# Optimization experiments

Hardware: AMD Instinct MI355X
Metric: run time of the kernel (lower is better)

The kernel has to match this reference:

```python
import jax, jax.numpy as jnp
import numpy as np

N, D, E, H, K = 16384, 256, 8, 512, 2


def setup_inputs() -> dict:
    key = jax.random.key(0)
    ks = jax.random.split(key, 5)
    inputs = jax.random.normal(ks[0], (N, D), dtype=jnp.float32)
    Wg = jax.random.normal(ks[1], (D, E), dtype=jnp.float32) * 0.05
    w1 = jax.random.normal(ks[2], (E, D, H), dtype=jnp.float32) * 0.05
    b1 = jnp.zeros((E, H), dtype=jnp.float32)
    w2 = jax.random.normal(ks[3], (E, H, D), dtype=jnp.float32) * 0.05
    b2 = jnp.zeros((E, D), dtype=jnp.float32)
    return {"inputs": inputs, "Wg": Wg, "w1": w1, "b1": b1, "w2": w2, "b2": b2}


def reference(inputs, Wg, w1, b1, w2, b2):
    # gate + top-k routing (softmax over the selected logits only, as in the torch code)
    gate_logits = inputs @ Wg                       # [N, E]
    topw, topi = jax.lax.top_k(gate_logits, K)      # [N, K]
    topw = jax.nn.softmax(topw.astype(jnp.float32), axis=1).astype(inputs.dtype)
    # combine weights scattered back into a dense [N, E] matrix (dispatch/combine)
    combine = jnp.zeros((N, E), dtype=inputs.dtype)
    combine = combine.at[jnp.arange(N)[:, None], topi].add(topw)  # [N, E]
    # expert MLP (Linear -> GELU(exact) -> Linear), computed per expert and
    # combined with the sparse routing weights (pool='sum')
    h = jax.nn.gelu(jnp.einsum('nd,edh->neh', inputs, w1) + b1[None], approximate=False)  # [N,E,H]
    y = jnp.einsum('neh,ehd->ned', h, w2) + b2[None]                                      # [N,E,D]
    return jnp.einsum('ne,ned->nd', combine, y)                                           # [N,D]
```

## Files before the change

### kernel.cpp

```cpp
#include <hip/hip_runtime.h>

#define NTOK 16384
#define DIM 256
#define NEXP 8
#define HID 512
#define CAP 5120
#define CSTRIDE 16

typedef unsigned short ushort_t;
typedef short bf16x8 __attribute__((ext_vector_type(8)));
typedef float f32x4 __attribute__((ext_vector_type(4)));

static __device__ __forceinline__ ushort_t f2bf(float f) {
    unsigned int u = __float_as_uint(f);
    unsigned int r = (u + 0x7FFFu + ((u >> 16) & 1u)) >> 16;
    return (ushort_t)r;
}
static __device__ __forceinline__ float bf2f(ushort_t u) {
    unsigned int x = ((unsigned int)u) << 16;
    return __uint_as_float(x);
}
static __device__ __forceinline__ float gelu_fast(float v) {
    float v2 = v * v;
    float u = v * __builtin_fmaf(v2, -0.1029407079f, -2.3022090196f);
    float e = __builtin_amdgcn_exp2f(u);
    return v * __builtin_amdgcn_rcpf(1.0f + e);
}

__global__ void k_transpose(const float* __restrict__ w1, const float* __restrict__ w2,
                            ushort_t* __restrict__ w1t, ushort_t* __restrict__ w2t,
                            int* __restrict__ counts) {
    __shared__ ushort_t tile[64][72];
    if (blockIdx.x == 0 && threadIdx.x < NEXP * CSTRIDE) counts[threadIdx.x] = 0;
    int b = blockIdx.x;
    const float* src; ushort_t* dst; int R, C, e, t;
    if (b < 256) { e = b >> 5; t = b & 31; src = w1; dst = w1t + e * DIM * HID; R = DIM; C = HID; }
    else { b -= 256; e = b >> 5; t = b & 31; src = w2; dst = w2t + e * DIM * HID; R = HID; C = DIM; }
    size_t ebase = (size_t)e * DIM * HID;
    int tilesC = C >> 6;
    int rt = t / tilesC, ct = t % tilesC;
    for (int i = 0; i < 16; i++) {
        int flat = i * 256 + threadIdx.x;
        int lr = flat >> 6, lc = flat & 63;
        tile[lr][lc] = f2bf(src[ebase + (size_t)(rt * 64 + lr) * C + ct * 64 + lc]);
    }
    __syncthreads();
    for (int i = 0; i < 16; i++) {
        int flat = i * 256 + threadIdx.x;
        int lr = flat >> 6, lc = flat & 63;
        dst[(ct * 64 + lr) * R + rt * 64 + lc] = tile[lc][lr];
    }
}

__global__ void k_router(const float* __restrict__ X, const float* __restrict__ Wg,
                         int* counts, int* tok_list, int* inv_idx, float* inv_w,
                         ushort_t* __restrict__ Xb) {
    __shared__ float xs[64][257];
    __shared__ float lg[64][8];
    __shared__ int te0[64], te1[64], lo0[64], lo1[64];
    __shared__ float tw0[64], tw1[64];
    __shared__ int lcnt[NEXP], gbase[NEXP];
    int tid = threadIdx.x;
    int tok0 = blockIdx.x * 64;
    if (tid < NEXP) lcnt[tid] = 0;
    for (int i = 0; i < 8; i++) {
        int flat = i * 256 + tid;
        int r = flat >> 5, c8 = (flat & 31) << 3;
        const float* row = X + (size_t)(tok0 + r) * DIM + c8;
        float4 a = *(const float4*)row;
        float4 b = *(const float4*)(row + 4);
        xs[r][c8 + 0] = a.x; xs[r][c8 + 1] = a.y; xs[r][c8 + 2] = a.z; xs[r][c8 + 3] = a.w;
        xs[r][c8 + 4] = b.x; xs[r][c8 + 5] = b.y; xs[r][c8 + 6] = b.z; xs[r][c8 + 7] = b.w;
    }
    __syncthreads();
    for (int i = 0; i < 8; i++) {
        int flat = i * 256 + tid;
        int r = flat >> 5, c8 = (flat & 31) << 3;
        ushort_t pk[8];
#pragma unroll
        for (int j = 0; j < 8; j++) pk[j] = f2bf(xs[r][c8 + j]);
        *(int4*)(Xb + (size_t)(tok0 + r) * DIM + c8) = *(const int4*)pk;
    }
    int tl = tid & 63, pair = tid >> 6;
    float l0 = 0.f, l1 = 0.f;
    for (int d = 0; d < DIM; d++) {
        float x = xs[tl][d];
        l0 += x * Wg[d * NEXP + 2 * pair];
        l1 += x * Wg[d * NEXP + 2 * pair + 1];
    }
    lg[tl][2 * pair] = l0; lg[tl][2 * pair + 1] = l1;
    __syncthreads();
    if (tid < 64) {
        float best = -1e30f; int bi = 0;
#pragma unroll
        for (int e = 0; e < NEXP; e++) { float v = lg[tid][e]; if (v > best) { best = v; bi = e; } }
        float best2 = -1e30f; int bi2 = 0;
#pragma unroll
        for (int e = 0; e < NEXP; e++) { if (e == bi) continue; float v = lg[tid][e]; if (v > best2) { best2 = v; bi2 = e; } }
        float ed = __expf(best2 - best);
        te0[tid] = bi; te1[tid] = bi2;
        tw0[tid] = 1.0f / (1.0f + ed);
        tw1[tid] = ed / (1.0f + ed);
        lo0[tid] = atomicAdd(&lcnt[bi], 1);
        lo1[tid] = atomicAdd(&lcnt[bi2], 1);
    }
    __syncthreads();
    if (tid < NEXP) gbase[tid] = atomicAdd(&counts[tid * CSTRIDE], lcnt[tid]);
    __syncthreads();
    if (tid < 64) {
        int token = tok0 + tid;
        int e0 = te0[tid], e1 = te1[tid];
        int p0 = gbase[e0] + lo0[tid]; if (p0 >= CAP) p0 = CAP - 1;
        int p1 = gbase[e1] + lo1[tid]; if (p1 >= CAP) p1 = CAP - 1;
        tok_list[e0 * CAP + p0] = token;
        tok_list[e1 * CAP + p1] = token;
        inv_idx[token * 2]     = (e0 << 16) | p0;  inv_w[token * 2]     = tw0[tid];
        inv_idx[token * 2 + 1] = (e1 << 16) | p1;  inv_w[token * 2 + 1] = tw1[tid];
    }
}

__launch_bounds__(512, 4)
__global__ void k_mlp1(const ushort_t* __restrict__ Xb, const ushort_t* __restrict__ w1t,
                       const float* __restrict__ b1,
                       const int* __restrict__ counts, const int* __restrict__ tok_list,
                       ushort_t* __restrict__ hb) {
    __shared__ ushort_t B1[128 * 264];
    int b = blockIdx.x;
    int e = b / 160;
    int rem = b % 160;
    int hq = rem / 40, tile = rem % 40;
    int count = counts[e * CSTRIDE];
    if (count > CAP) count = CAP;
    int t0 = tile * 128;
    if (t0 >= count) return;

    int tid = threadIdx.x;
    int w = tid >> 6, l = tid & 63, ln = l & 15, q = l >> 4;

    const ushort_t* w1te = w1t + (size_t)e * DIM * HID + (size_t)hq * 128 * DIM;
#pragma unroll
    for (int i = 0; i < 8; i++) {
        int flat = i * 512 + tid;
        int hr = flat >> 5, c8 = (flat & 31) << 3;
        *(int4*)(B1 + hr * 264 + c8) = *(const int4*)(w1te + hr * DIM + c8);
    }
    int arow = t0 + 16 * w + ln;
    int ci = (arow < count) ? arow : (count - 1);
    int atok = tok_list[e * CAP + ci];
    const ushort_t* xrow = Xb + (size_t)atok * DIM;
    bf16x8 xf[8];
#pragma unroll
    for (int ks = 0; ks < 8; ks++)
        xf[ks] = *(const bf16x8*)(xrow + ks * 32 + q * 8);
    __syncthreads();

    f32x4 zf = {0.f, 0.f, 0.f, 0.f};
    f32x4 acc[8];
#pragma unroll
    for (int i = 0; i < 8; i++) acc[i] = zf;
#pragma unroll
    for (int ks = 0; ks < 8; ks++) {
        bf16x8 xk = xf[ks];
#pragma unroll
        for (int cf = 0; cf < 8; cf++) {
            bf16x8 wfr = *(const bf16x8*)(B1 + (cf * 16 + ln) * 264 + ks * 32 + q * 8);
            acc[cf] = __builtin_amdgcn_mfma_f32_16x16x32_bf16(wfr, xk, acc[cf], 0, 0, 0);
        }
    }
    size_t hrowbase = ((size_t)e * CAP + t0 + 16 * w + ln) * HID + hq * 128;
#pragma unroll
    for (int cf = 0; cf < 8; cf++) {
        float4 bv = *(const float4*)(b1 + e * HID + hq * 128 + cf * 16 + q * 4);
        ushort4 pk;
        pk.x = f2bf(gelu_fast(acc[cf][0] + bv.x));
        pk.y = f2bf(gelu_fast(acc[cf][1] + bv.y));
        pk.z = f2bf(gelu_fast(acc[cf][2] + bv.z));
        pk.w = f2bf(gelu_fast(acc[cf][3] + bv.w));
        *(ushort4*)(hb + hrowbase + cf * 16 + q * 4) = pk;
    }
}

__launch_bounds__(512, 2)
__global__ void k_mlp2(const ushort_t* __restrict__ hb, const ushort_t* __restrict__ w2t,
                       const float* __restrict__ b2,
                       const int* __restrict__ counts, ushort_t* __restrict__ yb) {
    __shared__ ushort_t B2[64 * 520];
    int b = blockIdx.x;
    int e = b / 160;
    int rem = b % 160;
    int dq = rem / 40, tile = rem % 40;
    int count = counts[e * CSTRIDE];
    if (count > CAP) count = CAP;
    int t0 = tile * 128;
    if (t0 >= count) return;

    int tid = threadIdx.x;
    int w = tid >> 6, l = tid & 63, ln = l & 15, q = l >> 4;

    const ushort_t* w2te = w2t + (size_t)e * DIM * HID + (size_t)dq * 64 * HID;
#pragma unroll
    for (int i = 0; i < 8; i++) {
        int flat = i * 512 + tid;
        int dr = flat >> 6, c8 = (flat & 63) << 3;
        *(int4*)(B2 + dr * 520 + c8) = *(const int4*)(w2te + dr * HID + c8);
    }
    int arow = t0 + 16 * w + ln;
    int ci = (arow < count) ? arow : (count - 1);
    const ushort_t* hrow = hb + ((size_t)e * CAP + ci) * HID;
    bf16x8 af[16];
#pragma unroll
    for (int ks = 0; ks < 16; ks++)
        af[ks] = *(const bf16x8*)(hrow + ks * 32 + q * 8);
    __syncthreads();

    f32x4 zf = {0.f, 0.f, 0.f, 0.f};
    f32x4 acc[4];
#pragma unroll
    for (int i = 0; i < 4; i++) acc[i] = zf;
#pragma unroll
    for (int ks = 0; ks < 16; ks++) {
        bf16x8 hk = af[ks];
#pragma unroll
        for (int cf = 0; cf < 4; cf++) {
            bf16x8 wfr = *(const bf16x8*)(B2 + (cf * 16 + ln) * 520 + ks * 32 + q * 8);
            acc[cf] = __builtin_amdgcn_mfma_f32_16x16x32_bf16(wfr, hk, acc[cf], 0, 0, 0);
        }
    }
    size_t yrowbase = ((size_t)e * CAP + t0 + 16 * w + ln) * DIM + dq * 64;
#pragma unroll
    for (int cf = 0; cf < 4; cf++) {
        float4 bv = *(const float4*)(b2 + e * DIM + dq * 64 + cf * 16 + q * 4);
        ushort4 pk;
        pk.x = f2bf(acc[cf][0] + bv.x);
        pk.y = f2bf(acc[cf][1] + bv.y);
        pk.z = f2bf(acc[cf][2] + bv.z);
        pk.w = f2bf(acc[cf][3] + bv.w);
        *(ushort4*)(yb + yrowbase + cf * 16 + q * 4) = pk;
    }
}

__global__ void k_combine(const ushort_t* __restrict__ yb, const int* __restrict__ inv_idx,
                          const float* __restrict__ inv_w, float* __restrict__ out) {
    int tid = threadIdx.x;
    int n = blockIdx.x * 8 + (tid >> 5);
    int l32 = tid & 31, c8 = l32 << 3;
    int i0 = inv_idx[2 * n], i1 = inv_idx[2 * n + 1];
    float w0 = inv_w[2 * n], w1 = inv_w[2 * n + 1];
    size_t r0 = (size_t)(i0 >> 16) * CAP + (i0 & 0xFFFF);
    size_t r1 = (size_t)(i1 >> 16) * CAP + (i1 & 0xFFFF);
    int4 v0 = *(const int4*)(yb + r0 * DIM + c8);
    int4 v1 = *(const int4*)(yb + r1 * DIM + c8);
    ushort_t* p0 = (ushort_t*)&v0;
    ushort_t* p1 = (ushort_t*)&v1;
    float4 oa, ob;
    oa.x = w0 * bf2f(p0[0]) + w1 * bf2f(p1[0]);
    oa.y = w0 * bf2f(p0[1]) + w1 * bf2f(p1[1]);
    oa.z = w0 * bf2f(p0[2]) + w1 * bf2f(p1[2]);
    oa.w = w0 * bf2f(p0[3]) + w1 * bf2f(p1[3]);
    ob.x = w0 * bf2f(p0[4]) + w1 * bf2f(p1[4]);
    ob.y = w0 * bf2f(p0[5]) + w1 * bf2f(p1[5]);
    ob.z = w0 * bf2f(p0[6]) + w1 * bf2f(p1[6]);
    ob.w = w0 * bf2f(p0[7]) + w1 * bf2f(p1[7]);
    float4* op = (float4*)(out + (size_t)n * DIM + c8);
    op[0] = oa; op[1] = ob;
}

extern "C" void kernel_launch(void* const* d_in, const int* in_sizes, int n_in,
                              void* d_out, int out_size, void* d_ws, size_t ws_size,
                              hipStream_t stream) {
    const float* X  = (const float*)d_in[0];
    const float* Wg = (const float*)d_in[1];
    const float* w1 = (const float*)d_in[2];
    const float* b1 = (const float*)d_in[3];
    const float* w2 = (const float*)d_in[4];
    const float* b2 = (const float*)d_in[5];

    char* ws = (char*)d_ws;
    size_t off = 0;
    int* counts = (int*)(ws + off);        off = 1024;
    int* tok_list = (int*)(ws + off);      off += (size_t)NEXP * CAP * 4;
    int* inv_idx = (int*)(ws + off);       off += (size_t)NTOK * 2 * 4;
    float* inv_w = (float*)(ws + off);     off += (size_t)NTOK * 2 * 4;
    ushort_t* w1t = (ushort_t*)(ws + off); off += (size_t)NEXP * DIM * HID * 2;
    ushort_t* w2t = (ushort_t*)(ws + off); off += (size_t)NEXP * DIM * HID * 2;
    ushort_t* Xb = (ushort_t*)(ws + off);  off += (size_t)NTOK * DIM * 2;
    ushort_t* hb = (ushort_t*)(ws + off);  off += (size_t)NEXP * CAP * HID * 2;
    ushort_t* yb = (ushort_t*)(ws + off);  off += (size_t)NEXP * CAP * DIM * 2;

    k_transpose<<<512, 256, 0, stream>>>(w1, w2, w1t, w2t, counts);
    k_router<<<256, 256, 0, stream>>>(X, Wg, counts, tok_list, inv_idx, inv_w, Xb);
    k_mlp1<<<NEXP * 40 * 4, 512, 0, stream>>>(Xb, w1t, b1, counts, tok_list, hb);
    k_mlp2<<<NEXP * 40 * 4, 512, 0, stream>>>(hb, w2t, b2, counts, yb);
    k_combine<<<2048, 256, 0, stream>>>(yb, inv_idx, inv_w, (float*)d_out);
}
```

Before: 158.9 us.

## Fuse weight transpose into router kernel and halve mlp1 hidden tile

Merges the weight transpose/convert kernel and the router kernel into one launch, with block index selecting the role, and moves the counts reset to a memset. This removes one kernel boundary and lets transpose and routing blocks run concurrently. Separately, k_mlp1 now computes 64 hidden columns per block instead of 128, doubling the grid and halving LDS per block to raise occupancy. The cost is that each token row is re-read by twice as many blocks. The fused kernel also uses a large shared buffer for all blocks, which may limit occupancy for the transpose blocks.

```diff
diff --git a/kernel.cpp b/kernel.cpp
--- a/kernel.cpp
+++ b/kernel.cpp
@@ -27,40 +27,45 @@
     return v * __builtin_amdgcn_rcpf(1.0f + e);
 }
 
-__global__ void k_transpose(const float* __restrict__ w1, const float* __restrict__ w2,
-                            ushort_t* __restrict__ w1t, ushort_t* __restrict__ w2t,
-                            int* __restrict__ counts) {
-    __shared__ ushort_t tile[64][72];
-    if (blockIdx.x == 0 && threadIdx.x < NEXP * CSTRIDE) counts[threadIdx.x] = 0;
-    int b = blockIdx.x;
-    const float* src; ushort_t* dst; int R, C, e, t;
-    if (b < 256) { e = b >> 5; t = b & 31; src = w1; dst = w1t + e * DIM * HID; R = DIM; C = HID; }
-    else { b -= 256; e = b >> 5; t = b & 31; src = w2; dst = w2t + e * DIM * HID; R = HID; C = DIM; }
-    size_t ebase = (size_t)e * DIM * HID;
-    int tilesC = C >> 6;
-    int rt = t / tilesC, ct = t % tilesC;
-    for (int i = 0; i < 16; i++) {
-        int flat = i * 256 + threadIdx.x;
-        int lr = flat >> 6, lc = flat & 63;
-        tile[lr][lc] = f2bf(src[ebase + (size_t)(rt * 64 + lr) * C + ct * 64 + lc]);
-    }
-    __syncthreads();
-    for (int i = 0; i < 16; i++) {
-        int flat = i * 256 + threadIdx.x;
-        int lr = flat >> 6, lc = flat & 63;
-        dst[(ct * 64 + lr) * R + rt * 64 + lc] = tile[lc][lr];
-    }
-}
-
-__global__ void k_router(const float* __restrict__ X, const float* __restrict__ Wg,
-                         int* counts, int* tok_list, int* inv_idx, float* inv_w,
-                         ushort_t* __restrict__ Xb) {
-    __shared__ float xs[64][257];
-    __shared__ float lg[64][8];
-    __shared__ int te0[64], te1[64], lo0[64], lo1[64];
-    __shared__ float tw0[64], tw1[64];
-    __shared__ int lcnt[NEXP], gbase[NEXP];
+__global__ void k_prep(const float* __restrict__ X, const float* __restrict__ Wg,
+                       const float* __restrict__ w1, const float* __restrict__ w2,
+                       int* counts, int* tok_list, int* inv_idx, float* inv_w,
+                       ushort_t* __restrict__ Xb,
+                       ushort_t* __restrict__ w1t, ushort_t* __restrict__ w2t) {
+    __shared__ __align__(16) char smem[69504];
     int tid = threadIdx.x;
+    if (blockIdx.x >= 256) {
+        ushort_t (*tile)[72] = (ushort_t(*)[72])smem;
+        int b = blockIdx.x - 256;
+        const float* src; ushort_t* dst; int R, C, e, t;
+        if (b < 256) { e = b >> 5; t = b & 31; src = w1; dst = w1t + e * DIM * HID; R = DIM; C = HID; }
+        else { b -= 256; e = b >> 5; t = b & 31; src = w2; dst = w2t + e * DIM * HID; R = HID; C = DIM; }
+        size_t ebase = (size_t)e * DIM * HID;
+        int tilesC = C >> 6;
+        int rt = t / tilesC, ct = t % tilesC;
+        for (int i = 0; i < 16; i++) {
+            int flat = i * 256 + tid;
+            int lr = flat >> 6, lc = flat & 63;
+            tile[lr][lc] = f2bf(src[ebase + (size_t)(rt * 64 + lr) * C + ct * 64 + lc]);
+        }
+        __syncthreads();
+        for (int i = 0; i < 16; i++) {
+            int flat = i * 256 + tid;
+            int lr = flat >> 6, lc = flat & 63;
+            dst[(ct * 64 + lr) * R + rt * 64 + lc] = tile[lc][lr];
+        }
+        return;
+    }
+    float (*xs)[257] = (float(*)[257])smem;
+    float (*lg)[8] = (float(*)[8])(smem + 65792);
+    int* te0 = (int*)(smem + 67840);
+    int* te1 = (int*)(smem + 68096);
+    int* lo0 = (int*)(smem + 68352);
+    int* lo1 = (int*)(smem + 68608);
+    float* tw0 = (float*)(smem + 68864);
+    float* tw1 = (float*)(smem + 69120);
+    int* lcnt = (int*)(smem + 69376);
+    int* gbase = (int*)(smem + 69408);
     int tok0 = blockIdx.x * 64;
     if (tid < NEXP) lcnt[tid] = 0;
     for (int i = 0; i < 8; i++) {
@@ -124,10 +129,10 @@
                        const float* __restrict__ b1,
                        const int* __restrict__ counts, const int* __restrict__ tok_list,
                        ushort_t* __restrict__ hb) {
-    __shared__ ushort_t B1[128 * 264];
+    __shared__ ushort_t B1[64 * 264];
     int b = blockIdx.x;
-    int e = b / 160;
-    int rem = b % 160;
+    int e = b / 320;
+    int rem = b % 320;
     int hq = rem / 40, tile = rem % 40;
     int count = counts[e * CSTRIDE];
     if (count > CAP) count = CAP;
@@ -137,9 +142,9 @@
     int tid = threadIdx.x;
     int w = tid >> 6, l = tid & 63, ln = l & 15, q = l >> 4;
 
-    const ushort_t* w1te = w1t + (size_t)e * DIM * HID + (size_t)hq * 128 * DIM;
-#pragma unroll
-    for (int i = 0; i < 8; i++) {
+    const ushort_t* w1te = w1t + (size_t)e * DIM * HID + (size_t)hq * 64 * DIM;
+#pragma unroll
+    for (int i = 0; i < 4; i++) {
         int flat = i * 512 + tid;
         int hr = flat >> 5, c8 = (flat & 31) << 3;
         *(int4*)(B1 + hr * 264 + c8) = *(const int4*)(w1te + hr * DIM + c8);
@@ -155,22 +160,22 @@
     __syncthreads();
 
     f32x4 zf = {0.f, 0.f, 0.f, 0.f};
-    f32x4 acc[8];
-#pragma unroll
-    for (int i = 0; i < 8; i++) acc[i] = zf;
+    f32x4 acc[4];
+#pragma unroll
+    for (int i = 0; i < 4; i++) acc[i] = zf;
 #pragma unroll
     for (int ks = 0; ks < 8; ks++) {
         bf16x8 xk = xf[ks];
 #pragma unroll
-        for (int cf = 0; cf < 8; cf++) {
+        for (int cf = 0; cf < 4; cf++) {
             bf16x8 wfr = *(const bf16x8*)(B1 + (cf * 16 + ln) * 264 + ks * 32 + q * 8);
             acc[cf] = __builtin_amdgcn_mfma_f32_16x16x32_bf16(wfr, xk, acc[cf], 0, 0, 0);
         }
     }
-    size_t hrowbase = ((size_t)e * CAP + t0 + 16 * w + ln) * HID + hq * 128;
-#pragma unroll
-    for (int cf = 0; cf < 8; cf++) {
-        float4 bv = *(const float4*)(b1 + e * HID + hq * 128 + cf * 16 + q * 4);
+    size_t hrowbase = ((size_t)e * CAP + t0 + 16 * w + ln) * HID + hq * 64;
+#pragma unroll
+    for (int cf = 0; cf < 4; cf++) {
+        float4 bv = *(const float4*)(b1 + e * HID + hq * 64 + cf * 16 + q * 4);
         ushort4 pk;
         pk.x = f2bf(gelu_fast(acc[cf][0] + bv.x));
         pk.y = f2bf(gelu_fast(acc[cf][1] + bv.y));
@@ -287,9 +292,9 @@
     ushort_t* hb = (ushort_t*)(ws + off);  off += (size_t)NEXP * CAP * HID * 2;
     ushort_t* yb = (ushort_t*)(ws + off);  off += (size_t)NEXP * CAP * DIM * 2;
 
-    k_transpose<<<512, 256, 0, stream>>>(w1, w2, w1t, w2t, counts);
-    k_router<<<256, 256, 0, stream>>>(X, Wg, counts, tok_list, inv_idx, inv_w, Xb);
-    k_mlp1<<<NEXP * 40 * 4, 512, 0, stream>>>(Xb, w1t, b1, counts, tok_list, hb);
+    hipMemsetAsync(counts, 0, 1024, stream);
+    k_prep<<<768, 256, 0, stream>>>(X, Wg, w1, w2, counts, tok_list, inv_idx, inv_w, Xb, w1t, w2t);
+    k_mlp1<<<NEXP * 40 * 8, 512, 0, stream>>>(Xb, w1t, b1, counts, tok_list, hb);
     k_mlp2<<<NEXP * 40 * 4, 512, 0, stream>>>(hb, w2t, b2, counts, yb);
     k_combine<<<2048, 256, 0, stream>>>(yb, inv_idx, inv_w, (float*)d_out);
 }
```

Result: no change. 161.1 us (+1.4%).
